# Optimization experiments

Measured on AMD Instinct MI355X. Metric: run time of the kernel, lower is better.

## Reference

```python
import jax, jax.numpy as jnp
import numpy as np
from functools import partial

B, T, D_IN, H, D_OUT = 64, 2048, 256, 256, 128


def setup_inputs() -> dict:
    key = jax.random.key(0)
    ks = jax.random.split(key, 12)
    w = lambda k, shape: (jax.random.normal(k, shape, jnp.float32) * 0.05)
    inp = {
        "h": jax.random.normal(ks[0], (B, T, D_IN), jnp.float32),
        # linear_h_a: Linear(input_dim, hidden_dim, bias=False)
        "W_h_a": w(ks[1], (H, D_IN)),
        # linear_s_a: Linear(hidden_dim, hidden_dim, bias=True)
        "W_s_a": w(ks[2], (H, H)),
        "b_s_a": w(ks[3], (H,)),
        # linear_a: Linear(2*hidden_dim, 1, bias=False)
        "W_a": w(ks[4], (1, 2 * H)),
        # linear_init_s: Linear(input_dim, hidden_dim, bias=True)
        "W_init": w(ks[5], (H, D_IN)),
        "b_init": w(ks[6], (H,)),
        # GRUCell(output_dim+input_dim, hidden_dim); input is cat((ci, yim)) -> (D_IN + D_OUT)
        "W_ih_g": w(ks[7], (3 * H, D_IN + D_OUT)),
        "W_hh_g": w(ks[8], (3 * H, H)),
        "b_ih_g": jnp.zeros((3 * H,), jnp.float32),
        "b_hh_g": jnp.zeros((3 * H,), jnp.float32),
        # RNNCell(hidden_dim+input_dim, output_dim); input is cat((ci, si)) -> (D_IN + H)
        "W_ih_r": w(ks[9], (D_OUT, D_IN + H)),
        "W_hh_r": w(ks[10], (D_OUT, D_OUT)),
        "b_ih_r": jnp.zeros((D_OUT,), jnp.float32),
        "b_hh_r": jnp.zeros((D_OUT,), jnp.float32),
        "out_len": 64,
    }
    return inp


def _gru_cell(x, hp, W_ih, W_hh, b_ih, b_hh):
    gi = x @ W_ih.T + b_ih
    gh = hp @ W_hh.T + b_hh
    i_r, i_z, i_n = jnp.split(gi, 3, axis=1)
    h_r, h_z, h_n = jnp.split(gh, 3, axis=1)
    r = jax.nn.sigmoid(i_r + h_r)
    z = jax.nn.sigmoid(i_z + h_z)
    n = jnp.tanh(i_n + r * h_n)
    return (1.0 - z) * n + z * hp


def _rnn_cell(x, hp, W_ih, W_hh, b_ih, b_hh):
    return jnp.tanh(x @ W_ih.T + b_ih + hp @ W_hh.T + b_hh)


def _decode(h, W_h_a, W_s_a, b_s_a, W_a, W_init, b_init,
            W_ih_g, W_hh_g, b_ih_g, b_hh_g,
            W_ih_r, W_hh_r, b_ih_r, b_hh_r, out_len):
    # wh = linear_h_a(h): (B, T, H)
    wh = jnp.einsum("btd,hd->bth", h, W_h_a)
    # tanh(cat(wh, sa)) is elementwise, so the concat+linear_a splits exactly:
    # score = tanh(wh) @ W_a[:H] + tanh(sa) @ W_a[H:]
    wa1 = W_a[0, :W_s_a.shape[0]]
    wa2 = W_a[0, W_s_a.shape[0]:]
    twh = jnp.tanh(wh) @ wa1                       # (B, T) precomputed once

    s0 = jnp.tanh(h[:, 0, :] @ W_init.T + b_init)  # initHidden
    y0 = jnp.zeros((h.shape[0], W_ih_r.shape[0]), h.dtype)  # initSeq

    def step(carry, _):
        s, y = carry
        sa = jnp.tanh(s @ W_s_a.T + b_s_a) @ wa2   # (B,)
        a = jax.nn.softmax(twh + sa[:, None], axis=1)      # (B, T)
        ci = jnp.einsum("bt,btd->bd", a, h)                # context (B, D_in)
        si = _gru_cell(jnp.concatenate([ci, y], axis=1), s,
                       W_ih_g, W_hh_g, b_ih_g, b_hh_g)
        yi = jax.nn.softmax(
            _rnn_cell(jnp.concatenate([ci, si], axis=1), y,
                      W_ih_r, W_hh_r, b_ih_r, b_hh_r), axis=1)
        return (si, yi), yi

    _, ys = jax.lax.scan(step, (s0, y0), None, length=out_len)
    return jnp.transpose(ys, (1, 0, 2))  # (B, out_len, D_out)


def reference(h, W_h_a, W_s_a, b_s_a, W_a, W_init, b_init,
              W_ih_g, W_hh_g, b_ih_g, b_hh_g,
              W_ih_r, W_hh_r, b_ih_r, b_hh_r, out_len):
    return _decode(h, W_h_a, W_s_a, b_s_a, W_a, W_init, b_init,
                   W_ih_g, W_hh_g, b_ih_g, b_hh_g,
                   W_ih_r, W_hh_r, b_ih_r, b_hh_r, out_len)
```

## Files before the change

kernel.cpp:

```cpp
#include <hip/hip_runtime.h>
#include <cstdint>

typedef unsigned short ushort_t;
typedef __attribute__((ext_vector_type(8))) short short8;
typedef __attribute__((ext_vector_type(4))) short short4_t;
typedef __attribute__((ext_vector_type(4))) float f4;

#define BB   64
#define TT   2048
#define DD   256
#define DO_  128
#define OL   64

#define O_TWH   0
#define O_RMAX  131072
#define O_RDEN  131136
#define O_CIP   131200
#define O_CI    393344
#define O_GIC   409728
#define O_RIC   458880
#define O_S0    467072
#define O_SG    483456
#define O_LP    516224
#define O_CTR   647296
#define O_RWS   647808
#define O_RWY   680576
#define O_US    696960
#define U_WB    0
#define U_BG    65536

static __device__ __forceinline__ ushort_t f2bf(float f) {
  union { float f; uint32_t u; } v; v.f = f;
  uint32_t u = v.u;
  u += 0x7FFFu + ((u >> 16) & 1u);
  return (ushort_t)(u >> 16);
}
static __device__ __forceinline__ uint32_t fbits(float f) {
  union { float f; uint32_t u; } v; v.f = f; return v.u;
}
static __device__ __forceinline__ float fast_tanh(float x) {
  float e = __expf(2.f * x);
  return 1.f - 2.f / (e + 1.f);
}
static __device__ __forceinline__ float fast_sigmoid(float x) {
  return 1.f / (1.f + __expf(-x));
}
static __device__ __forceinline__ void llc_store_tag(float* p, float v, uint32_t tag) {
  union { float f; uint32_t u; } x; x.f = v;
  x.u = (x.u & ~3u) | tag;
  __hip_atomic_store((uint32_t*)p, x.u, __ATOMIC_RELAXED, __HIP_MEMORY_SCOPE_AGENT);
}

__global__ __launch_bounds__(256) void k_prep(const float* __restrict__ Wha,
    const float* __restrict__ Whhg, const float* __restrict__ Wihg,
    const float* __restrict__ Wihr, const float* __restrict__ Whhr,
    float* __restrict__ ws, ushort_t* __restrict__ us) {
  int idx = blockIdx.x * 256 + threadIdx.x;
  if (idx < 65536) {
    us[U_WB + idx] = f2bf(Wha[idx]);
    return;
  }
  if (idx < 65536 + 294912) {
    int i = idx - 65536;
    int pos = i & 7;
    int l = (i >> 3) & 63;
    int r = i >> 9;
    int kb = r % 12;
    int r2 = r / 12;
    int n = r2 % 6;
    int blk = r2 / 6;
    int c = n * 16 + (l & 15);
    int g = c >> 5;
    int kl = c & 31;
    int kg = 32 * blk + kl;
    int j = kb * 32 + ((l >> 4) & 3) * 8 + pos;
    int row = g * 256 + kg;
    float v;
    if (j < 256) v = Whhg[row * 256 + j];
    else         v = Wihg[row * 384 + j];
    us[U_BG + i] = f2bf(v);
    return;
  }
  if (idx < 65536 + 294912 + 32768) {
    int i = idx - (65536 + 294912);
    int m = i & 127, kl = (i >> 7) & 31, blk = i >> 12;
    ws[O_RWS + i] = Wihr[m * 512 + 256 + 32 * blk + kl];
  } else {
    int i = idx - (65536 + 294912 + 32768);
    int m = i & 127, jl = (i >> 7) & 15, blk = i >> 11;
    ws[O_RWY + i] = Whhr[m * 128 + 16 * blk + jl];
  }
}

__global__ __launch_bounds__(256) void k_twh(const float* __restrict__ h,
                                             const ushort_t* __restrict__ Wb,
                                             const float* __restrict__ Wa,
                                             float* __restrict__ twh) {
  __shared__ __align__(16) ushort_t alds[64 * 264];
  __shared__ float walds[256];
  const int tid = threadIdx.x;
  const long rowbase = (long)blockIdx.x * 64;
  walds[tid] = Wa[tid];
  for (int it = 0; it < 8; ++it) {
    int q = it * 256 + tid;
    int r = q >> 5;
    int c8 = q & 31;
    const float* src = h + (rowbase + r) * 256 + c8 * 8;
    float4 a = *(const float4*)(src);
    float4 b = *(const float4*)(src + 4);
    union { ushort_t u[8]; short8 v; } t;
    t.u[0]=f2bf(a.x); t.u[1]=f2bf(a.y); t.u[2]=f2bf(a.z); t.u[3]=f2bf(a.w);
    t.u[4]=f2bf(b.x); t.u[5]=f2bf(b.y); t.u[6]=f2bf(b.z); t.u[7]=f2bf(b.w);
    *(short8*)&alds[r * 264 + c8 * 8] = t.v;
  }
  __syncthreads();
  const int l = tid & 63, w = tid >> 6;
  const int cres = l & 15, kg = l >> 4;
  f4 acc[16];
  #pragma unroll
  for (int f = 0; f < 16; ++f) acc[f] = (f4){0.f, 0.f, 0.f, 0.f};
  const int arow = 16 * w + cres;
  #pragma unroll
  for (int ks = 0; ks < 8; ++ks) {
    short8 af = *(const short8*)&alds[arow * 264 + ks * 32 + kg * 8];
    const ushort_t* bp = Wb + ks * 32 + kg * 8 + cres * 256;
    #pragma unroll
    for (int f = 0; f < 16; ++f) {
      short8 bf = *(const short8*)(bp + f * 16 * 256);
      acc[f] = __builtin_amdgcn_mfma_f32_16x16x32_bf16(af, bf, acc[f], 0, 0, 0);
    }
  }
  float t4[4] = {0.f, 0.f, 0.f, 0.f};
  #pragma unroll
  for (int f = 0; f < 16; ++f) {
    float wa = walds[16 * f + cres];
    #pragma unroll
    for (int r = 0; r < 4; ++r) t4[r] += fast_tanh(acc[f][r]) * wa;
  }
  #pragma unroll
  for (int m = 1; m <= 8; m <<= 1) {
    #pragma unroll
    for (int r = 0; r < 4; ++r) t4[r] += __shfl_xor(t4[r], m);
  }
  if (cres == 0) {
    #pragma unroll
    for (int r = 0; r < 4; ++r)
      twh[rowbase + 16 * w + kg * 4 + r] = t4[r];
  }
}

__global__ __launch_bounds__(256) void k_stats(const float* __restrict__ twh,
                                               float* __restrict__ rmax,
                                               float* __restrict__ rden) {
  __shared__ float redm[4], reds[4];
  const int b = blockIdx.x, tid = threadIdx.x;
  float v[8];
  #pragma unroll
  for (int j = 0; j < 8; ++j) v[j] = twh[b * 2048 + tid + j * 256];
  float mx = v[0];
  #pragma unroll
  for (int j = 1; j < 8; ++j) mx = fmaxf(mx, v[j]);
  #pragma unroll
  for (int d = 32; d >= 1; d >>= 1) mx = fmaxf(mx, __shfl_xor(mx, d));
  if ((tid & 63) == 0) redm[tid >> 6] = mx;
  __syncthreads();
  float M = fmaxf(fmaxf(redm[0], redm[1]), fmaxf(redm[2], redm[3]));
  float s = 0.f;
  #pragma unroll
  for (int j = 0; j < 8; ++j) s += __expf(v[j] - M);
  #pragma unroll
  for (int d = 32; d >= 1; d >>= 1) s += __shfl_xor(s, d);
  if ((tid & 63) == 0) reds[tid >> 6] = s;
  __syncthreads();
  if (tid == 0) { rmax[b] = M; rden[b] = reds[0] + reds[1] + reds[2] + reds[3]; }
}

__global__ __launch_bounds__(256) void k_cipart(const float* __restrict__ h,
                                                const float* __restrict__ twh,
                                                const float* __restrict__ rmax,
                                                float* __restrict__ cipart) {
  __shared__ float p[128];
  const int b = blockIdx.x >> 4, ts = blockIdx.x & 15;
  const int tid = threadIdx.x;
  const int t0 = ts * 128;
  if (tid < 128) p[tid] = __expf(twh[b * 2048 + t0 + tid] - rmax[b]);
  __syncthreads();
  float acc = 0.f;
  const float* hp = h + ((long)(b * 2048 + t0)) * 256 + tid;
  #pragma unroll 8
  for (int i = 0; i < 128; ++i) { acc += p[i] * hp[0]; hp += 256; }
  cipart[(b * 16 + ts) * 256 + tid] = acc;
}

__global__ __launch_bounds__(256) void k_cired(const float* __restrict__ cipart,
                                               const float* __restrict__ rden,
                                               float* __restrict__ ci) {
  const int b = blockIdx.x, d = threadIdx.x;
  float a = 0.f;
  #pragma unroll
  for (int ts = 0; ts < 16; ++ts) a += cipart[(b * 16 + ts) * 256 + d];
  ci[b * 256 + d] = a / rden[b];
}

__global__ __launch_bounds__(256) void k_const(const float* __restrict__ h,
    const float* __restrict__ ci,
    const float* __restrict__ Wihg, const float* __restrict__ bihg,
    const float* __restrict__ bhhg,
    const float* __restrict__ Wihr, const float* __restrict__ bihr,
    const float* __restrict__ bhhr,
    const float* __restrict__ Winit, const float* __restrict__ binit,
    float* __restrict__ gic, float* __restrict__ ric, float* __restrict__ s0) {
  __shared__ float cil[256], h0l[256];
  const int b = blockIdx.x, tid = threadIdx.x;
  cil[tid] = ci[b * 256 + tid];
  h0l[tid] = h[(long)b * 2048 * 256 + tid];
  __syncthreads();
  const int k = tid;
  #pragma unroll
  for (int g = 0; g < 3; ++g) {
    float a = bihg[g * 256 + k] + (g < 2 ? bhhg[g * 256 + k] : 0.f);
    const float* wp = Wihg + (long)(g * 256 + k) * 384;
    for (int d = 0; d < 256; d += 4) {
      float4 w4 = *(const float4*)(wp + d);
      a += cil[d] * w4.x + cil[d + 1] * w4.y + cil[d + 2] * w4.z + cil[d + 3] * w4.w;
    }
    gic[b * 768 + g * 256 + k] = a;
  }
  {
    float a = binit[k];
    const float* wp = Winit + (long)k * 256;
    for (int d = 0; d < 256; d += 4) {
      float4 w4 = *(const float4*)(wp + d);
      a += h0l[d] * w4.x + h0l[d + 1] * w4.y + h0l[d + 2] * w4.z + h0l[d + 3] * w4.w;
    }
    s0[b * 256 + k] = fast_tanh(a);
  }
  if (tid < 128) {
    int m = tid;
    float a = bihr[m] + bhhr[m];
    const float* wp = Wihr + (long)m * 512;
    for (int d = 0; d < 256; d += 4) {
      float4 w4 = *(const float4*)(wp + d);
      a += cil[d] * w4.x + cil[d + 1] * w4.y + cil[d + 2] * w4.z + cil[d + 3] * w4.w;
    }
    ric[b * 128 + m] = a;
  }
}

__global__ __launch_bounds__(512) void k_loop(
    const float* __restrict__ gic, const float* __restrict__ ric,
    const float* __restrict__ s0w, const float* __restrict__ bhhg,
    const ushort_t* __restrict__ BG, const float* __restrict__ RWSg,
    const float* __restrict__ RWYg,
    float* __restrict__ sg, float* __restrict__ lp,
    float* __restrict__ out) {
  __shared__ __align__(16) ushort_t Bl[36864];
  __shared__ __align__(16) ushort_t Al[6144];
  __shared__ float RWSl[32][128];
  __shared__ float RWYl[16][128];
  __shared__ float gsum[8][128];
  __shared__ float sslice[8][32];
  __shared__ float ybuf[8][128];
  __shared__ float ricl[8][128];
  __shared__ float gicl[8][3][32];
  __shared__ float bnl[32];
  const int tid = threadIdx.x;
  const int grp = blockIdx.x & 7;
  const int blk = blockIdx.x >> 3;
  const int b0 = grp * 8;

  {
    const short8* src = (const short8*)(BG + (long)blk * 36864);
    short8* dst = (short8*)Bl;
    for (int i = tid; i < 4608; i += 512) dst[i] = src[i];
  }
  for (int i = tid; i < 4096; i += 512) ((float*)RWSl)[i] = RWSg[blk * 4096 + i];
  for (int i = tid; i < 2048; i += 512) ((float*)RWYl)[i] = RWYg[blk * 2048 + i];
  for (int i = tid; i < 1024; i += 512) ((float*)ricl)[i] = ric[b0 * 128 + i];
  for (int i = tid; i < 768; i += 512) {
    int bb = i / 96, rem = i % 96, g = rem >> 5, kl = rem & 31;
    gicl[bb][g][kl] = gic[(b0 + bb) * 768 + g * 256 + blk * 32 + kl];
  }
  if (tid < 32) bnl[tid] = bhhg[512 + blk * 32 + tid];
  if (tid < 256) {
    int bb = tid >> 5, kl = tid & 31;
    sslice[bb][kl] = s0w[(b0 + bb) * 256 + blk * 32 + kl];
  }
  for (int i = tid; i < 1024; i += 512) ((float*)ybuf)[i] = 0.f;
  for (int i = tid; i < 3072; i += 512) {
    int kb = i >> 8, rem = i & 255, kg = rem >> 6, row = 8 + ((rem >> 3) & 7), pos = rem & 7;
    Al[((kb * 4 + kg) * 16 + row) * 8 + pos] = 0;
  }
  __syncthreads();

  for (int it = 0; it <= OL; ++it) {
    const int par = it & 1;
    const int bb1 = tid >> 6, ml = tid & 63;
    f4 sgv;
    if (it > 0) {
      const uint32_t texp = (((uint32_t)it) >> 1) & 3u;
      const float* aL = lp + (((long)((par * 8 + grp) * 8 + bb1)) << 10) + ml;
      const float* a2 = sg + par * 16384 + (b0 + bb1) * 256 + ml * 4;
      float r0,r1,r2,r3,r4,r5,r6,r7,r8,r9,r10,r11,r12,r13,r14,r15;
      while (true) {
        asm volatile(
          "global_load_dword %0, %17, off sc0 sc1\n\t"
          "global_load_dword %1, %17, off offset:512 sc0 sc1\n\t"
          "global_load_dword %2, %17, off offset:1024 sc0 sc1\n\t"
          "global_load_dword %3, %17, off offset:1536 sc0 sc1\n\t"
          "global_load_dword %4, %17, off offset:2048 sc0 sc1\n\t"
          "global_load_dword %5, %17, off offset:2560 sc0 sc1\n\t"
          "global_load_dword %6, %17, off offset:3072 sc0 sc1\n\t"
          "global_load_dword %7, %17, off offset:3584 sc0 sc1\n\t"
          "global_load_dword %8, %17, off offset:256 sc0 sc1\n\t"
          "global_load_dword %9, %17, off offset:768 sc0 sc1\n\t"
          "global_load_dword %10, %17, off offset:1280 sc0 sc1\n\t"
          "global_load_dword %11, %17, off offset:1792 sc0 sc1\n\t"
          "global_load_dword %12, %17, off offset:2304 sc0 sc1\n\t"
          "global_load_dword %13, %17, off offset:2816 sc0 sc1\n\t"
          "global_load_dword %14, %17, off offset:3328 sc0 sc1\n\t"
          "global_load_dword %15, %17, off offset:3840 sc0 sc1\n\t"
          "global_load_dwordx4 %16, %18, off sc0 sc1\n\t"
          "s_waitcnt vmcnt(0)"
          : "=&v"(r0), "=&v"(r1), "=&v"(r2), "=&v"(r3),
            "=&v"(r4), "=&v"(r5), "=&v"(r6), "=&v"(r7),
            "=&v"(r8), "=&v"(r9), "=&v"(r10), "=&v"(r11),
            "=&v"(r12), "=&v"(r13), "=&v"(r14), "=&v"(r15),
            "=&v"(sgv)
          : "v"(aL), "v"(a2)
          : "memory");
        uint32_t bad = (fbits(r0) ^ texp) | (fbits(r1) ^ texp) |
                       (fbits(r2) ^ texp) | (fbits(r3) ^ texp) |
                       (fbits(r4) ^ texp) | (fbits(r5) ^ texp) |
                       (fbits(r6) ^ texp) | (fbits(r7) ^ texp) |
                       (fbits(r8) ^ texp) | (fbits(r9) ^ texp) |
                       (fbits(r10) ^ texp) | (fbits(r11) ^ texp) |
                       (fbits(r12) ^ texp) | (fbits(r13) ^ texp) |
                       (fbits(r14) ^ texp) | (fbits(r15) ^ texp) |
                       (fbits(sgv[0]) ^ texp) | (fbits(sgv[1]) ^ texp) |
                       (fbits(sgv[2]) ^ texp) | (fbits(sgv[3]) ^ texp);
        if ((bad & 3u) == 0u) break;
        __builtin_amdgcn_s_sleep(1);
      }
      float L0 = ricl[bb1][ml]      + ((r0+r1)+(r2+r3)) + ((r4+r5)+(r6+r7));
      float L1 = ricl[bb1][ml + 64] + ((r8+r9)+(r10+r11)) + ((r12+r13)+(r14+r15));
      L0 = fast_tanh(L0); L1 = fast_tanh(L1);
      float e0 = __expf(L0), e1 = __expf(L1);
      float s = e0 + e1;
      #pragma unroll
      for (int d = 32; d >= 1; d >>= 1) s += __shfl_xor(s, d);
      float y0 = e0 / s, y1 = e1 / s;
      ybuf[bb1][ml] = y0; ybuf[bb1][ml + 64] = y1;
      if (bb1 == blk) {
        float* op = out + ((long)(b0 + blk) * OL + (it - 1)) * DO_;
        op[ml] = y0; op[ml + 64] = y1;
      }
    } else {
      sgv = *(const f4*)(s0w + (b0 + bb1) * 256 + ml * 4);
    }
    if (it == OL) break;
    __syncthreads();
    {
      const int j4 = ml * 4;
      int kb = j4 >> 5, kg = (j4 >> 3) & 3, pos = j4 & 7;
      short4_t h4;
      h4[0] = (short)f2bf(sgv[0]); h4[1] = (short)f2bf(sgv[1]);
      h4[2] = (short)f2bf(sgv[2]); h4[3] = (short)f2bf(sgv[3]);
      *(short4_t*)&Al[((kb * 4 + kg) * 16 + bb1) * 8 + pos] = h4;
    }
    if (tid < 256) {
      const int bb = tid >> 5, jl4 = (tid & 31) * 4;
      const int j = 256 + jl4;
      int kb = j >> 5, kg = (j >> 3) & 3, pos = j & 7;
      short4_t h4;
      h4[0] = (short)f2bf(ybuf[bb][jl4]);     h4[1] = (short)f2bf(ybuf[bb][jl4 + 1]);
      h4[2] = (short)f2bf(ybuf[bb][jl4 + 2]); h4[3] = (short)f2bf(ybuf[bb][jl4 + 3]);
      *(short4_t*)&Al[((kb * 4 + kg) * 16 + bb) * 8 + pos] = h4;
    }
    __syncthreads();
    if (tid < 128) {
      const int w = tid >> 6, l = tid & 63;
      f4 a0 = (f4){0,0,0,0}, a1 = (f4){0,0,0,0}, a2v = (f4){0,0,0,0};
      f4 m1 = (f4){0,0,0,0}, m2 = (f4){0,0,0,0};
      const short8* Ap = (const short8*)Al + l;
      const short8* Bp = (const short8*)Bl + (w * 3) * 768 + l;
      #pragma unroll
      for (int kb = 0; kb < 12; ++kb) {
        short8 af = Ap[kb * 64];
        a0 = __builtin_amdgcn_mfma_f32_16x16x32_bf16(af, Bp[kb * 64], a0, 0, 0, 0);
        a1 = __builtin_amdgcn_mfma_f32_16x16x32_bf16(af, Bp[768 + kb * 64], a1, 0, 0, 0);
        a2v = __builtin_amdgcn_mfma_f32_16x16x32_bf16(af, Bp[1536 + kb * 64], a2v, 0, 0, 0);
        if (kb == 7) { m1 = a1; m2 = a2v; }
      }
      if (l < 32) {
        const int bbase = (l >> 4) * 4, c = l & 15;
        if (w == 0) {
          #pragma unroll
          for (int r = 0; r < 4; ++r) {
            gsum[bbase + r][c]      = a0[r];
            gsum[bbase + r][16 + c] = a1[r];
            gsum[bbase + r][32 + c] = a2v[r];
          }
        } else {
          #pragma unroll
          for (int r = 0; r < 4; ++r) {
            gsum[bbase + r][48 + c] = a0[r];
            gsum[bbase + r][64 + c]      = m1[r];
            gsum[bbase + r][96 + c]      = a1[r] - m1[r];
            gsum[bbase + r][64 + 16 + c] = m2[r];
            gsum[bbase + r][96 + 16 + c] = a2v[r] - m2[r];
          }
        }
      }
    }
    __syncthreads();
    {
      const uint32_t tprod = (((uint32_t)it + 1u) >> 1) & 3u;
      if (tid < 256) {
        const int bb = tid >> 5, kl = tid & 31;
        float sold = sslice[bb][kl];
        float R   = fast_sigmoid(gsum[bb][kl]      + gicl[bb][0][kl]);
        float Z   = fast_sigmoid(gsum[bb][32 + kl] + gicl[bb][1][kl]);
        float hn  = gsum[bb][64 + kl] + bnl[kl];
        float in_ = gsum[bb][96 + kl] + gicl[bb][2][kl];
        float N = fast_tanh(in_ + R * hn);
        float sn = (1.f - Z) * N + Z * sold;
        sslice[bb][kl] = sn;
        llc_store_tag(sg + (par ^ 1) * 16384 + (b0 + bb) * 256 + blk * 32 + kl, sn, tprod);
      }
    }
    __syncthreads();
    {
      const uint32_t tprod = (((uint32_t)it + 1u) >> 1) & 3u;
      const int m = tid & 127, q = tid >> 7;
      const int ba = 2 * q, bbv = 2 * q + 1;
      float acc0 = 0.f, acc1 = 0.f;
      #pragma unroll 8
      for (int kl = 0; kl < 32; ++kl) {
        float w = RWSl[kl][m];
        acc0 += w * sslice[ba][kl];
        acc1 += w * sslice[bbv][kl];
      }
      #pragma unroll 8
      for (int jl = 0; jl < 16; ++jl) {
        float w = RWYl[jl][m];
        acc0 += w * ybuf[ba][16 * blk + jl];
        acc1 += w * ybuf[bbv][16 * blk + jl];
      }
      float* dst = lp + (((long)((par ^ 1) * 8 + grp) * 8) << 10) + blk * 128 + m;
      llc_store_tag(dst + (ba  << 10), acc0, tprod);
      llc_store_tag(dst + (bbv << 10), acc1, tprod);
    }
    __syncthreads();
  }
}

extern "C" void kernel_launch(void* const* d_in, const int* in_sizes, int n_in,
                              void* d_out, int out_size, void* d_ws, size_t ws_size,
                              hipStream_t stream) {
  const float* h     = (const float*)d_in[0];
  const float* Wha   = (const float*)d_in[1];
  const float* Wa    = (const float*)d_in[4];
  const float* Winit = (const float*)d_in[5];
  const float* binit = (const float*)d_in[6];
  const float* Wihg  = (const float*)d_in[7];
  const float* Whhg  = (const float*)d_in[8];
  const float* bihg  = (const float*)d_in[9];
  const float* bhhg  = (const float*)d_in[10];
  const float* Wihr  = (const float*)d_in[11];
  const float* Whhr  = (const float*)d_in[12];
  const float* bihr  = (const float*)d_in[13];
  const float* bhhr  = (const float*)d_in[14];
  float* ws  = (float*)d_ws;
  float* out = (float*)d_out;
  ushort_t* us = (ushort_t*)(ws + O_US);

  hipMemsetAsync((char*)d_ws + (size_t)O_SG * 4,             0x00, 16384 * 4, stream);
  hipMemsetAsync((char*)d_ws + (size_t)(O_SG + 16384) * 4,   0xFF, 16384 * 4, stream);
  hipMemsetAsync((char*)d_ws + (size_t)O_LP * 4,             0x00, 65536 * 4, stream);
  hipMemsetAsync((char*)d_ws + (size_t)(O_LP + 65536) * 4,   0xFF, 65536 * 4, stream);

  k_prep<<<dim3(1600), dim3(256), 0, stream>>>(Wha, Whhg, Wihg, Wihr, Whhr, ws, us);
  k_twh<<<dim3(2048), dim3(256), 0, stream>>>(h, us + U_WB, Wa, ws + O_TWH);
  k_stats<<<dim3(64), dim3(256), 0, stream>>>(ws + O_TWH, ws + O_RMAX, ws + O_RDEN);
  k_cipart<<<dim3(1024), dim3(256), 0, stream>>>(h, ws + O_TWH, ws + O_RMAX, ws + O_CIP);
  k_cired<<<dim3(64), dim3(256), 0, stream>>>(ws + O_CIP, ws + O_RDEN, ws + O_CI);
  k_const<<<dim3(64), dim3(256), 0, stream>>>(h, ws + O_CI, Wihg, bihg, bhhg,
                                              Wihr, bihr, bhhr, Winit, binit,
                                              ws + O_GIC, ws + O_RIC, ws + O_S0);
  k_loop<<<dim3(64), dim3(512), 0, stream>>>(ws + O_GIC, ws + O_RIC, ws + O_S0, bhhg,
                                             us + U_BG, ws + O_RWS, ws + O_RWY,
                                             ws + O_SG, ws + O_LP,
                                             out);
}
```

Before: 452.9 us.

## Fuse softmax stats into context kernel, merge reduction into const kernel, fold memsets

Four memset calls are replaced by stores inside the prep kernel, removing separate launches. The row-max/denominator kernel is fused into the context-partial kernel: each block recomputes the row max and emits a partial denominator. The partial reduction is merged into the constants kernel, which now stages weights through shared memory for coalesced loads. k_twh stages the bf16 weight tile in LDS per k-step instead of loading it directly from global memory. Together these cut kernel launches and serial small kernels, at the cost of redundant max computation and extra barriers.

```diff
diff --git a/kernel.cpp b/kernel.cpp
--- a/kernel.cpp
+++ b/kernel.cpp
@@ -13,16 +13,13 @@
 #define OL   64
 
 #define O_TWH   0
-#define O_RMAX  131072
-#define O_RDEN  131136
-#define O_CIP   131200
-#define O_CI    393344
+#define O_PDEN  131072
+#define O_CIP   132096
 #define O_GIC   409728
 #define O_RIC   458880
 #define O_S0    467072
 #define O_SG    483456
 #define O_LP    516224
-#define O_CTR   647296
 #define O_RWS   647808
 #define O_RWY   680576
 #define O_US    696960
@@ -49,6 +46,9 @@
   union { float f; uint32_t u; } x; x.f = v;
   x.u = (x.u & ~3u) | tag;
   __hip_atomic_store((uint32_t*)p, x.u, __ATOMIC_RELAXED, __HIP_MEMORY_SCOPE_AGENT);
+}
+static __device__ __forceinline__ void llc_store_u32(uint32_t* p, uint32_t v) {
+  __hip_atomic_store(p, v, __ATOMIC_RELAXED, __HIP_MEMORY_SCOPE_AGENT);
 }
 
 __global__ __launch_bounds__(256) void k_prep(const float* __restrict__ Wha,
@@ -85,10 +85,22 @@
     int i = idx - (65536 + 294912);
     int m = i & 127, kl = (i >> 7) & 31, blk = i >> 12;
     ws[O_RWS + i] = Wihr[m * 512 + 256 + 32 * blk + kl];
-  } else {
+    return;
+  }
+  if (idx < 65536 + 294912 + 32768 + 16384) {
     int i = idx - (65536 + 294912 + 32768);
     int m = i & 127, jl = (i >> 7) & 15, blk = i >> 11;
     ws[O_RWY + i] = Whhr[m * 128 + 16 * blk + jl];
+    return;
+  }
+  if (idx < 409600 + 32768) {
+    int i = idx - 409600;
+    llc_store_u32((uint32_t*)(ws + O_SG) + i, (i < 16384) ? 0u : 0xFFFFFFFFu);
+    return;
+  }
+  {
+    int i = idx - (409600 + 32768);
+    llc_store_u32((uint32_t*)(ws + O_LP) + i, (i < 65536) ? 0u : 0xFFFFFFFFu);
   }
 }
 
@@ -97,6 +109,7 @@
                                              const float* __restrict__ Wa,
                                              float* __restrict__ twh) {
   __shared__ __align__(16) ushort_t alds[64 * 264];
+  __shared__ __align__(16) ushort_t blds[256 * 40];
   __shared__ float walds[256];
   const int tid = threadIdx.x;
   const long rowbase = (long)blockIdx.x * 64;
@@ -120,15 +133,21 @@
   #pragma unroll
   for (int f = 0; f < 16; ++f) acc[f] = (f4){0.f, 0.f, 0.f, 0.f};
   const int arow = 16 * w + cres;
-  #pragma unroll
   for (int ks = 0; ks < 8; ++ks) {
+    #pragma unroll
+    for (int i = 0; i < 4; ++i) {
+      int lin = i * 256 + tid;
+      int r = lin >> 2, c8 = (lin & 3) * 8;
+      *(short8*)&blds[r * 40 + c8] = *(const short8*)(Wb + r * 256 + ks * 32 + c8);
+    }
+    __syncthreads();
     short8 af = *(const short8*)&alds[arow * 264 + ks * 32 + kg * 8];
-    const ushort_t* bp = Wb + ks * 32 + kg * 8 + cres * 256;
     #pragma unroll
     for (int f = 0; f < 16; ++f) {
-      short8 bf = *(const short8*)(bp + f * 16 * 256);
+      short8 bf = *(const short8*)&blds[(f * 16 + cres) * 40 + kg * 8];
       acc[f] = __builtin_amdgcn_mfma_f32_16x16x32_bf16(af, bf, acc[f], 0, 0, 0);
     }
+    __syncthreads();
   }
   float t4[4] = {0.f, 0.f, 0.f, 0.f};
   #pragma unroll
@@ -149,11 +168,15 @@
   }
 }
 
-__global__ __launch_bounds__(256) void k_stats(const float* __restrict__ twh,
-                                               float* __restrict__ rmax,
-                                               float* __restrict__ rden) {
-  __shared__ float redm[4], reds[4];
-  const int b = blockIdx.x, tid = threadIdx.x;
+__global__ __launch_bounds__(256) void k_cipart2(const float* __restrict__ h,
+                                                 const float* __restrict__ twh,
+                                                 float* __restrict__ cipart,
+                                                 float* __restrict__ pden) {
+  __shared__ float p[128];
+  __shared__ float redm[4];
+  __shared__ float redd[2];
+  const int b = blockIdx.x >> 4, ts = blockIdx.x & 15;
+  const int tid = threadIdx.x;
   float v[8];
   #pragma unroll
   for (int j = 0; j < 8; ++j) v[j] = twh[b * 2048 + tid + j * 256];
@@ -165,45 +188,25 @@
   if ((tid & 63) == 0) redm[tid >> 6] = mx;
   __syncthreads();
   float M = fmaxf(fmaxf(redm[0], redm[1]), fmaxf(redm[2], redm[3]));
-  float s = 0.f;
-  #pragma unroll
-  for (int j = 0; j < 8; ++j) s += __expf(v[j] - M);
-  #pragma unroll
-  for (int d = 32; d >= 1; d >>= 1) s += __shfl_xor(s, d);
-  if ((tid & 63) == 0) reds[tid >> 6] = s;
+  if ((tid >> 7) == (ts & 1)) p[tid & 127] = __expf(v[ts >> 1] - M);
   __syncthreads();
-  if (tid == 0) { rmax[b] = M; rden[b] = reds[0] + reds[1] + reds[2] + reds[3]; }
-}
-
-__global__ __launch_bounds__(256) void k_cipart(const float* __restrict__ h,
-                                                const float* __restrict__ twh,
-                                                const float* __restrict__ rmax,
-                                                float* __restrict__ cipart) {
-  __shared__ float p[128];
-  const int b = blockIdx.x >> 4, ts = blockIdx.x & 15;
-  const int tid = threadIdx.x;
-  const int t0 = ts * 128;
-  if (tid < 128) p[tid] = __expf(twh[b * 2048 + t0 + tid] - rmax[b]);
+  if (tid < 128) {
+    float e = p[tid];
+    #pragma unroll
+    for (int d = 32; d >= 1; d >>= 1) e += __shfl_xor(e, d);
+    if ((tid & 63) == 0) redd[tid >> 6] = e;
+  }
   __syncthreads();
+  if (tid == 0) pden[b * 16 + ts] = redd[0] + redd[1];
   float acc = 0.f;
-  const float* hp = h + ((long)(b * 2048 + t0)) * 256 + tid;
+  const float* hp = h + ((long)(b * 2048 + ts * 128)) * 256 + tid;
   #pragma unroll 8
   for (int i = 0; i < 128; ++i) { acc += p[i] * hp[0]; hp += 256; }
   cipart[(b * 16 + ts) * 256 + tid] = acc;
 }
 
-__global__ __launch_bounds__(256) void k_cired(const float* __restrict__ cipart,
-                                               const float* __restrict__ rden,
-                                               float* __restrict__ ci) {
-  const int b = blockIdx.x, d = threadIdx.x;
-  float a = 0.f;
-  #pragma unroll
-  for (int ts = 0; ts < 16; ++ts) a += cipart[(b * 16 + ts) * 256 + d];
-  ci[b * 256 + d] = a / rden[b];
-}
-
-__global__ __launch_bounds__(256) void k_const(const float* __restrict__ h,
-    const float* __restrict__ ci,
+__global__ __launch_bounds__(256) void k_cc(const float* __restrict__ h,
+    const float* __restrict__ cipart, const float* __restrict__ pden,
     const float* __restrict__ Wihg, const float* __restrict__ bihg,
     const float* __restrict__ bhhg,
     const float* __restrict__ Wihr, const float* __restrict__ bihr,
@@ -211,39 +214,68 @@
     const float* __restrict__ Winit, const float* __restrict__ binit,
     float* __restrict__ gic, float* __restrict__ ric, float* __restrict__ s0) {
   __shared__ float cil[256], h0l[256];
+  __shared__ float wt[256][33];
   const int b = blockIdx.x, tid = threadIdx.x;
-  cil[tid] = ci[b * 256 + tid];
-  h0l[tid] = h[(long)b * 2048 * 256 + tid];
+  {
+    float a = 0.f;
+    #pragma unroll
+    for (int ts = 0; ts < 16; ++ts) a += cipart[(b * 16 + ts) * 256 + tid];
+    float den = 0.f;
+    #pragma unroll
+    for (int ts = 0; ts < 16; ++ts) den += pden[b * 16 + ts];
+    cil[tid] = a / den;
+    h0l[tid] = h[(long)b * 2048 * 256 + tid];
+  }
   __syncthreads();
-  const int k = tid;
-  #pragma unroll
   for (int g = 0; g < 3; ++g) {
-    float a = bihg[g * 256 + k] + (g < 2 ? bhhg[g * 256 + k] : 0.f);
-    const float* wp = Wihg + (long)(g * 256 + k) * 384;
-    for (int d = 0; d < 256; d += 4) {
-      float4 w4 = *(const float4*)(wp + d);
-      a += cil[d] * w4.x + cil[d + 1] * w4.y + cil[d + 2] * w4.z + cil[d + 3] * w4.w;
-    }
-    gic[b * 768 + g * 256 + k] = a;
+    float acc = bihg[g * 256 + tid] + (g < 2 ? bhhg[g * 256 + tid] : 0.f);
+    for (int d0 = 0; d0 < 256; d0 += 32) {
+      __syncthreads();
+      #pragma unroll
+      for (int i = 0; i < 32; ++i) {
+        int lin = i * 256 + tid;
+        int k = lin >> 5, dd = lin & 31;
+        wt[k][dd] = Wihg[(g * 256 + k) * 384 + d0 + dd];
+      }
+      __syncthreads();
+      #pragma unroll
+      for (int dd = 0; dd < 32; ++dd) acc += cil[d0 + dd] * wt[tid][dd];
+    }
+    gic[b * 768 + g * 256 + tid] = acc;
   }
   {
-    float a = binit[k];
-    const float* wp = Winit + (long)k * 256;
-    for (int d = 0; d < 256; d += 4) {
-      float4 w4 = *(const float4*)(wp + d);
-      a += h0l[d] * w4.x + h0l[d + 1] * w4.y + h0l[d + 2] * w4.z + h0l[d + 3] * w4.w;
-    }
-    s0[b * 256 + k] = fast_tanh(a);
-  }
-  if (tid < 128) {
-    int m = tid;
-    float a = bihr[m] + bhhr[m];
-    const float* wp = Wihr + (long)m * 512;
-    for (int d = 0; d < 256; d += 4) {
-      float4 w4 = *(const float4*)(wp + d);
-      a += cil[d] * w4.x + cil[d + 1] * w4.y + cil[d + 2] * w4.z + cil[d + 3] * w4.w;
-    }
-    ric[b * 128 + m] = a;
+    float acc = binit[tid];
+    for (int d0 = 0; d0 < 256; d0 += 32) {
+      __syncthreads();
+      #pragma unroll
+      for (int i = 0; i < 32; ++i) {
+        int lin = i * 256 + tid;
+        int k = lin >> 5, dd = lin & 31;
+        wt[k][dd] = Winit[k * 256 + d0 + dd];
+      }
+      __syncthreads();
+      #pragma unroll
+      for (int dd = 0; dd < 32; ++dd) acc += h0l[d0 + dd] * wt[tid][dd];
+    }
+    s0[b * 256 + tid] = fast_tanh(acc);
+  }
+  {
+    float acc = (tid < 128) ? (bihr[tid] + bhhr[tid]) : 0.f;
+    for (int d0 = 0; d0 < 256; d0 += 32) {
+      __syncthreads();
+      #pragma unroll
+      for (int i = 0; i < 16; ++i) {
+        int lin = i * 256 + tid;
+        int m = lin >> 5, dd = lin & 31;
+        wt[m][dd] = Wihr[m * 512 + d0 + dd];
+      }
+      __syncthreads();
+      if (tid < 128) {
+        #pragma unroll
+        for (int dd = 0; dd < 32; ++dd) acc += cil[d0 + dd] * wt[tid][dd];
+      }
+    }
+    if (tid < 128) ric[b * 128 + tid] = acc;
   }
 }
 
@@ -475,19 +507,13 @@
   float* out = (float*)d_out;
   ushort_t* us = (ushort_t*)(ws + O_US);
 
-  hipMemsetAsync((char*)d_ws + (size_t)O_SG * 4,             0x00, 16384 * 4, stream);
-  hipMemsetAsync((char*)d_ws + (size_t)(O_SG + 16384) * 4,   0xFF, 16384 * 4, stream);
-  hipMemsetAsync((char*)d_ws + (size_t)O_LP * 4,             0x00, 65536 * 4, stream);
-  hipMemsetAsync((char*)d_ws + (size_t)(O_LP + 65536) * 4,   0xFF, 65536 * 4, stream);
-
-  k_prep<<<dim3(1600), dim3(256), 0, stream>>>(Wha, Whhg, Wihg, Wihr, Whhr, ws, us);
+  k_prep<<<dim3(2240), dim3(256), 0, stream>>>(Wha, Whhg, Wihg, Wihr, Whhr, ws, us);
   k_twh<<<dim3(2048), dim3(256), 0, stream>>>(h, us + U_WB, Wa, ws + O_TWH);
-  k_stats<<<dim3(64), dim3(256), 0, stream>>>(ws + O_TWH, ws + O_RMAX, ws + O_RDEN);
-  k_cipart<<<dim3(1024), dim3(256), 0, stream>>>(h, ws + O_TWH, ws + O_RMAX, ws + O_CIP);
-  k_cired<<<dim3(64), dim3(256), 0, stream>>>(ws + O_CIP, ws + O_RDEN, ws + O_CI);
-  k_const<<<dim3(64), dim3(256), 0, stream>>>(h, ws + O_CI, Wihg, bihg, bhhg,
-                                              Wihr, bihr, bhhr, Winit, binit,
-                                              ws + O_GIC, ws + O_RIC, ws + O_S0);
+  k_cipart2<<<dim3(1024), dim3(256), 0, stream>>>(h, ws + O_TWH, ws + O_CIP, ws + O_PDEN);
+  k_cc<<<dim3(64), dim3(256), 0, stream>>>(h, ws + O_CIP, ws + O_PDEN,
+                                           Wihg, bihg, bhhg, Wihr, bihr, bhhr,
+                                           Winit, binit,
+                                           ws + O_GIC, ws + O_RIC, ws + O_S0);
   k_loop<<<dim3(64), dim3(512), 0, stream>>>(ws + O_GIC, ws + O_RIC, ws + O_S0, bhhg,
                                              us + U_BG, ws + O_RWS, ws + O_RWY,
                                              ws + O_SG, ws + O_LP,
```

Result: faster. 403.4 us, median of 2 (-10.9%).
